# Optimization experiments

Hardware: AMD Instinct MI355X
Metric: run time of the kernel (lower is better)

The kernel has to match this reference:

```python
import jax, jax.numpy as jnp
import numpy as np

B, T = 256, 2048
VOCAB, EMB, HID, OUT = 7, 20, 128, 6


def setup_inputs() -> dict:
    key = jax.random.key(0)
    ks = jax.random.split(key, 9)
    s_ih = 1.0 / np.sqrt(HID)
    inp = {
        "inputs": jax.random.randint(ks[0], (B, T), 0, VOCAB),
        "c0": jax.random.normal(ks[1], (1, B, HID), dtype=jnp.float32),
        # PyTorch LSTM params (gate order i,f,g,o), uniform(-1/sqrt(H), 1/sqrt(H))
        "W_ih": jax.random.uniform(ks[2], (4 * HID, EMB), jnp.float32, -s_ih, s_ih),
        "W_hh": jax.random.uniform(ks[3], (4 * HID, HID), jnp.float32, -s_ih, s_ih),
        "b_ih": jax.random.uniform(ks[4], (4 * HID,), jnp.float32, -s_ih, s_ih),
        "b_hh": jax.random.uniform(ks[5], (4 * HID,), jnp.float32, -s_ih, s_ih),
        "W_fc": jax.random.uniform(ks[6], (OUT, HID), jnp.float32, -s_ih, s_ih),
        "b_fc": jax.random.uniform(ks[7], (OUT,), jnp.float32, -s_ih, s_ih),
        "emb": jax.random.normal(ks[8], (VOCAB, EMB), dtype=jnp.float32),
    }
    return inp


def _lstm(x_gates, h0, c0, W_hh):
    # x_gates: [T, B, 4H] precomputed input contributions (+ both biases)
    def step(carry, xg):
        h, c = carry
        gates = xg + h @ W_hh.T  # [B, 4H]
        i, f, g, o = jnp.split(gates, 4, axis=-1)
        i, f, o = jax.nn.sigmoid(i), jax.nn.sigmoid(f), jax.nn.sigmoid(o)
        g = jnp.tanh(g)
        c = f * c + i * g
        h = o * jnp.tanh(c)
        return (h, c), h

    (_, _), hs = jax.lax.scan(step, (h0, c0), x_gates)
    return hs  # [T, B, H]


def reference(inputs, c0, W_ih, W_hh, b_ih, b_hh, W_fc, b_fc, emb):
    x = emb[inputs]  # [B, T, EMB]
    # precompute input-to-gate projection once (batched GEMM)
    x_gates = jnp.einsum("bte,ge->btg", x, W_ih) + (b_ih + b_hh)  # [B,T,4H]
    x_gates = jnp.transpose(x_gates, (1, 0, 2))  # [T, B, 4H]
    h0 = jnp.zeros((B, HID), dtype=x.dtype)
    hs = _lstm(x_gates, h0, c0[0], W_hh)  # [T, B, H]
    hiddens = jnp.transpose(hs, (1, 0, 2))  # [B, T, H]
    logits = jnp.einsum("bth,oh->bto", hiddens, W_fc) + b_fc
    return jax.nn.softmax(logits, axis=2)
```

## Files before the change

### kernel.cpp

```cpp
#include <hip/hip_runtime.h>
#include <math.h>

#define BB 256
#define TT 2048
#define VOCAB 7
#define EMBD 20
#define HID 128
#define OUTD 6
#define CHUNK 64
#define NCHUNK (TT / CHUNK)

typedef _Float16 h2 __attribute__((ext_vector_type(2)));

__device__ __forceinline__ float v_exp2(float x) {
    float r; asm("v_exp_f32 %0, %1" : "=v"(r) : "v"(x)); return r;
}
__device__ __forceinline__ float v_rcp(float x) {
    float r; asm("v_rcp_f32 %0, %1" : "=v"(r) : "v"(x)); return r;
}
__device__ __forceinline__ float sigmoid_f(float x) {
    return v_rcp(1.0f + v_exp2(-1.44269504f * x));
}
__device__ __forceinline__ float tanh_f(float x) {
    float ax = fabsf(x);
    float t = v_exp2(-2.88539008f * ax);
    float r = (1.0f - t) * v_rcp(1.0f + t);
    return __builtin_copysignf(r, x);
}

__device__ __forceinline__ float dot2(h2 a, h2 b, float c) {
    float d;
    asm("v_dot2_f32_f16 %0, %1, %2, %3" : "=v"(d) : "v"(a), "v"(b), "v"(c));
    return d;
}

#define KEEP(x) asm volatile("" : "+v"(x))

__global__ __launch_bounds__(512) void lstm_persist(
    const int* __restrict__ inputs, const float* __restrict__ c0,
    const float* __restrict__ W_ih, const float* __restrict__ W_hh,
    const float* __restrict__ b_ih, const float* __restrict__ b_hh,
    const float* __restrict__ W_fc, const float* __restrict__ b_fc,
    const float* __restrict__ emb, float* __restrict__ out)
{
    __shared__ float4   gtab[VOCAB][HID];
    __shared__ _Float16 hbuf[CHUNK][HID];
    __shared__ int      toks[CHUNK];
    __shared__ float    ldspad[24 * 1024];

    const int tid  = threadIdx.x;
    const int b    = blockIdx.x;
    const int j    = tid >> 2;
    const int r    = tid & 3;
    const int lane = tid & 63;
    const int wave = tid >> 6;

    h2 w0[16], w1[16], w2[16], w3[16];
    {
        const float2* p0 = (const float2*)(W_hh + ((size_t)(0 * HID + j) * HID + r * 32));
        const float2* p1 = (const float2*)(W_hh + ((size_t)(1 * HID + j) * HID + r * 32));
        const float2* p2 = (const float2*)(W_hh + ((size_t)(2 * HID + j) * HID + r * 32));
        const float2* p3 = (const float2*)(W_hh + ((size_t)(3 * HID + j) * HID + r * 32));
        #pragma unroll
        for (int k = 0; k < 16; ++k) {
            float2 f0 = p0[k], f1 = p1[k], f2 = p2[k], f3 = p3[k];
            h2 a; a.x = (_Float16)f0.x; a.y = (_Float16)f0.y; w0[k] = a;
            h2 bq; bq.x = (_Float16)f1.x; bq.y = (_Float16)f1.y; w1[k] = bq;
            h2 cq; cq.x = (_Float16)f2.x; cq.y = (_Float16)f2.y; w2[k] = cq;
            h2 dq; dq.x = (_Float16)f3.x; dq.y = (_Float16)f3.y; w3[k] = dq;
        }
    }
    #pragma unroll
    for (int k = 0; k < 16; ++k) { KEEP(w0[k]); KEEP(w1[k]); KEEP(w2[k]); KEEP(w3[k]); }

    {
        const int g = r * HID + j;
        float wih[EMBD];
        #pragma unroll
        for (int e = 0; e < EMBD; ++e) wih[e] = W_ih[g * EMBD + e];
        float bb = b_ih[g] + b_hh[g];
        #pragma unroll
        for (int v = 0; v < VOCAB; ++v) {
            float a = bb;
            #pragma unroll
            for (int e = 0; e < EMBD; ++e) a += wih[e] * emb[v * EMBD + e];
            ((float*)&gtab[v][j])[r] = a;
        }
    }

    float c = c0[b * HID + j];
    if (tid < HID) hbuf[CHUNK - 1][tid] = (_Float16)0.f;

    float wfc0[OUTD], wfc1[OUTD], bfc[OUTD];
    #pragma unroll
    for (int o = 0; o < OUTD; ++o) {
        wfc0[o] = W_fc[o * HID + 2 * lane];
        wfc1[o] = W_fc[o * HID + 2 * lane + 1];
        bfc[o]  = b_fc[o];
    }
    __syncthreads();

    #pragma unroll 1
    for (int ch = 0; ch < NCHUNK; ++ch) {
        const int t0 = ch * CHUNK;
        if (tid < CHUNK) toks[tid] = inputs[(size_t)b * TT + t0 + tid];
        __syncthreads();

        #pragma unroll 1
        for (int s = 0; s < CHUNK; ++s) {
            const int prev = (s + CHUNK - 1) & (CHUNK - 1);

            const uint4* hp = (const uint4*)&hbuf[prev][r * 32];
            float a0 = 0.f, a1 = 0.f, a2 = 0.f, a3 = 0.f;
            #pragma unroll
            for (int k = 0; k < 4; ++k) {
                uint4 v = hp[k];
                h2 hx = __builtin_bit_cast(h2, v.x);
                h2 hy = __builtin_bit_cast(h2, v.y);
                h2 hz = __builtin_bit_cast(h2, v.z);
                h2 hw = __builtin_bit_cast(h2, v.w);
                a0 = dot2(w0[4*k+0], hx, a0); a0 = dot2(w0[4*k+1], hy, a0);
                a0 = dot2(w0[4*k+2], hz, a0); a0 = dot2(w0[4*k+3], hw, a0);
                a1 = dot2(w1[4*k+0], hx, a1); a1 = dot2(w1[4*k+1], hy, a1);
                a1 = dot2(w1[4*k+2], hz, a1); a1 = dot2(w1[4*k+3], hw, a1);
                a2 = dot2(w2[4*k+0], hx, a2); a2 = dot2(w2[4*k+1], hy, a2);
                a2 = dot2(w2[4*k+2], hz, a2); a2 = dot2(w2[4*k+3], hw, a2);
                a3 = dot2(w3[4*k+0], hx, a3); a3 = dot2(w3[4*k+1], hy, a3);
                a3 = dot2(w3[4*k+2], hz, a3); a3 = dot2(w3[4*k+3], hw, a3);
            }
            a0 += __shfl_xor(a0, 1, 64); a0 += __shfl_xor(a0, 2, 64);
            a1 += __shfl_xor(a1, 1, 64); a1 += __shfl_xor(a1, 2, 64);
            a2 += __shfl_xor(a2, 1, 64); a2 += __shfl_xor(a2, 2, 64);
            a3 += __shfl_xor(a3, 1, 64); a3 += __shfl_xor(a3, 2, 64);

            const float4 xg = gtab[toks[s]][j];
            float gi = sigmoid_f(a0 + xg.x);
            float gf = sigmoid_f(a1 + xg.y);
            float gg = tanh_f  (a2 + xg.z);
            float go = sigmoid_f(a3 + xg.w);
            c = gf * c + gi * gg;
            float h = go * tanh_f(c);
            if (r == 0) hbuf[s][j] = (_Float16)h;
            __syncthreads();
        }

        #pragma unroll 1
        for (int i = 0; i < CHUNK / 8; ++i) {
            const int row = wave * (CHUNK / 8) + i;
            h2 hv = ((const h2*)&hbuf[row][0])[lane];
            float h0 = (float)hv.x, h1 = (float)hv.y;
            float acc[OUTD];
            #pragma unroll
            for (int o = 0; o < OUTD; ++o) acc[o] = wfc0[o] * h0 + wfc1[o] * h1;
            #pragma unroll
            for (int off = 32; off >= 1; off >>= 1) {
                #pragma unroll
                for (int o = 0; o < OUTD; ++o) acc[o] += __shfl_xor(acc[o], off, 64);
            }
            if (lane == 0) {
                float m = -1e30f;
                #pragma unroll
                for (int o = 0; o < OUTD; ++o) { acc[o] += bfc[o]; m = fmaxf(m, acc[o]); }
                float e[OUTD], ssum = 0.f;
                #pragma unroll
                for (int o = 0; o < OUTD; ++o) { e[o] = v_exp2(1.44269504f * (acc[o] - m)); ssum += e[o]; }
                float inv = v_rcp(ssum);
                float* po = out + ((size_t)b * TT + (t0 + row)) * OUTD;
                #pragma unroll
                for (int o = 0; o < OUTD; ++o) po[o] = e[o] * inv;
            }
        }
        __syncthreads();
    }

    if (__builtin_expect(inputs[0] == -2147483647, 0)) {
        volatile float* vp = ldspad;
        vp[tid] = (float)tid;
        out[tid] = vp[tid + 1];
    }
}

extern "C" void kernel_launch(void* const* d_in, const int* in_sizes, int n_in,
                              void* d_out, int out_size, void* d_ws, size_t ws_size,
                              hipStream_t stream) {
    const int*   inputs = (const int*)  d_in[0];
    const float* c0     = (const float*)d_in[1];
    const float* W_ih   = (const float*)d_in[2];
    const float* W_hh   = (const float*)d_in[3];
    const float* b_ih   = (const float*)d_in[4];
    const float* b_hh   = (const float*)d_in[5];
    const float* W_fc   = (const float*)d_in[6];
    const float* b_fc   = (const float*)d_in[7];
    const float* emb    = (const float*)d_in[8];
    float* out = (float*)d_out;

    lstm_persist<<<BB, 512, 0, stream>>>(inputs, c0, W_ih, W_hh, b_ih, b_hh,
                                         W_fc, b_fc, emb, out);
}
```

Before: 1.584 ms.

## Split each hidden unit's recurrent dot product across eight threads with 1024-thread blocks

Doubles the block to 1024 threads so each hidden unit's four gate dot products are split across eight lanes of 16 elements instead of four lanes of 32. This halves per-thread serial dot2 work and weight registers, at the cost of an extra shuffle-reduction stage and a costlier block-wide barrier every step. It also preloads all tokens into shared memory once and prefetches the next step's input-gate row before the barrier. The dot product now uses the fdot2 builtin instead of inline asm, and the padding array is halved.

Result: slower. 2.070 ms (+30.7%).

```diff
diff --git a/kernel.cpp b/kernel.cpp
--- a/kernel.cpp
+++ b/kernel.cpp
@@ -28,15 +28,21 @@
     return __builtin_copysignf(r, x);
 }
 
+#if defined(__has_builtin)
+#if __has_builtin(__builtin_amdgcn_fdot2)
+#define HAS_FDOT2 1
+#endif
+#endif
+
 __device__ __forceinline__ float dot2(h2 a, h2 b, float c) {
-    float d;
-    asm("v_dot2_f32_f16 %0, %1, %2, %3" : "=v"(d) : "v"(a), "v"(b), "v"(c));
-    return d;
-}
-
-#define KEEP(x) asm volatile("" : "+v"(x))
-
-__global__ __launch_bounds__(512) void lstm_persist(
+#ifdef HAS_FDOT2
+    return __builtin_amdgcn_fdot2(a, b, c, false);
+#else
+    return c + (float)a.x * (float)b.x + (float)a.y * (float)b.y;
+#endif
+}
+
+__global__ __launch_bounds__(1024) void lstm_persist(
     const int* __restrict__ inputs, const float* __restrict__ c0,
     const float* __restrict__ W_ih, const float* __restrict__ W_hh,
     const float* __restrict__ b_ih, const float* __restrict__ b_hh,
@@ -45,36 +51,35 @@
 {
     __shared__ float4   gtab[VOCAB][HID];
     __shared__ _Float16 hbuf[CHUNK][HID];
-    __shared__ int      toks[CHUNK];
-    __shared__ float    ldspad[24 * 1024];
+    __shared__ int      toks[TT];
+    __shared__ float    ldspad[12 * 1024];
 
     const int tid  = threadIdx.x;
     const int b    = blockIdx.x;
-    const int j    = tid >> 2;
-    const int r    = tid & 3;
+    const int j    = tid >> 3;
+    const int r    = tid & 7;
     const int lane = tid & 63;
     const int wave = tid >> 6;
 
-    h2 w0[16], w1[16], w2[16], w3[16];
-    {
-        const float2* p0 = (const float2*)(W_hh + ((size_t)(0 * HID + j) * HID + r * 32));
-        const float2* p1 = (const float2*)(W_hh + ((size_t)(1 * HID + j) * HID + r * 32));
-        const float2* p2 = (const float2*)(W_hh + ((size_t)(2 * HID + j) * HID + r * 32));
-        const float2* p3 = (const float2*)(W_hh + ((size_t)(3 * HID + j) * HID + r * 32));
+    toks[tid]        = inputs[(size_t)b * TT + tid];
+    toks[tid + 1024] = inputs[(size_t)b * TT + tid + 1024];
+
+    h2 w[4][8];
+    #pragma unroll
+    for (int g = 0; g < 4; ++g) {
+        const float2* wp = (const float2*)(W_hh + ((size_t)(g * HID + j) * HID + r * 16));
         #pragma unroll
-        for (int k = 0; k < 16; ++k) {
-            float2 f0 = p0[k], f1 = p1[k], f2 = p2[k], f3 = p3[k];
-            h2 a; a.x = (_Float16)f0.x; a.y = (_Float16)f0.y; w0[k] = a;
-            h2 bq; bq.x = (_Float16)f1.x; bq.y = (_Float16)f1.y; w1[k] = bq;
-            h2 cq; cq.x = (_Float16)f2.x; cq.y = (_Float16)f2.y; w2[k] = cq;
-            h2 dq; dq.x = (_Float16)f3.x; dq.y = (_Float16)f3.y; w3[k] = dq;
-        }
-    }
-    #pragma unroll
-    for (int k = 0; k < 16; ++k) { KEEP(w0[k]); KEEP(w1[k]); KEEP(w2[k]); KEEP(w3[k]); }
-
-    {
-        const int g = r * HID + j;
+        for (int k = 0; k < 8; ++k) {
+            float2 f = wp[k];
+            h2 p; p.x = (_Float16)f.x; p.y = (_Float16)f.y;
+            w[g][k] = p;
+        }
+    }
+
+    if (tid < 4 * HID) {
+        const int jj = tid & (HID - 1);
+        const int gg = tid >> 7;
+        const int g  = gg * HID + jj;
         float wih[EMBD];
         #pragma unroll
         for (int e = 0; e < EMBD; ++e) wih[e] = W_ih[g * EMBD + e];
@@ -84,7 +89,7 @@
             float a = bb;
             #pragma unroll
             for (int e = 0; e < EMBD; ++e) a += wih[e] * emb[v * EMBD + e];
-            ((float*)&gtab[v][j])[r] = a;
+            ((float*)&gtab[v][jj])[gg] = a;
         }
     }
 
@@ -100,40 +105,51 @@
     }
     __syncthreads();
 
+    float4 xg = gtab[toks[0]][j];
+
     #pragma unroll 1
     for (int ch = 0; ch < NCHUNK; ++ch) {
         const int t0 = ch * CHUNK;
-        if (tid < CHUNK) toks[tid] = inputs[(size_t)b * TT + t0 + tid];
-        __syncthreads();
 
         #pragma unroll 1
         for (int s = 0; s < CHUNK; ++s) {
+            const int t    = t0 + s;
             const int prev = (s + CHUNK - 1) & (CHUNK - 1);
 
-            const uint4* hp = (const uint4*)&hbuf[prev][r * 32];
+            const uint4* hp = (const uint4*)&hbuf[prev][r * 16];
+            uint4 v0 = hp[0], v1 = hp[1];
+
             float a0 = 0.f, a1 = 0.f, a2 = 0.f, a3 = 0.f;
             #pragma unroll
-            for (int k = 0; k < 4; ++k) {
-                uint4 v = hp[k];
-                h2 hx = __builtin_bit_cast(h2, v.x);
-                h2 hy = __builtin_bit_cast(h2, v.y);
-                h2 hz = __builtin_bit_cast(h2, v.z);
-                h2 hw = __builtin_bit_cast(h2, v.w);
-                a0 = dot2(w0[4*k+0], hx, a0); a0 = dot2(w0[4*k+1], hy, a0);
-                a0 = dot2(w0[4*k+2], hz, a0); a0 = dot2(w0[4*k+3], hw, a0);
-                a1 = dot2(w1[4*k+0], hx, a1); a1 = dot2(w1[4*k+1], hy, a1);
-                a1 = dot2(w1[4*k+2], hz, a1); a1 = dot2(w1[4*k+3], hw, a1);
-                a2 = dot2(w2[4*k+0], hx, a2); a2 = dot2(w2[4*k+1], hy, a2);
-                a2 = dot2(w2[4*k+2], hz, a2); a2 = dot2(w2[4*k+3], hw, a2);
-                a3 = dot2(w3[4*k+0], hx, a3); a3 = dot2(w3[4*k+1], hy, a3);
-                a3 = dot2(w3[4*k+2], hz, a3); a3 = dot2(w3[4*k+3], hw, a3);
+            for (int g = 0; g < 1; ++g) {  }
+            {
+                h2 hx0 = __builtin_bit_cast(h2, v0.x), hy0 = __builtin_bit_cast(h2, v0.y);
+                h2 hz0 = __builtin_bit_cast(h2, v0.z), hw0 = __builtin_bit_cast(h2, v0.w);
+                h2 hx1 = __builtin_bit_cast(h2, v1.x), hy1 = __builtin_bit_cast(h2, v1.y);
+                h2 hz1 = __builtin_bit_cast(h2, v1.z), hw1 = __builtin_bit_cast(h2, v1.w);
+                a0 = dot2(w[0][0], hx0, a0); a0 = dot2(w[0][1], hy0, a0);
+                a0 = dot2(w[0][2], hz0, a0); a0 = dot2(w[0][3], hw0, a0);
+                a0 = dot2(w[0][4], hx1, a0); a0 = dot2(w[0][5], hy1, a0);
+                a0 = dot2(w[0][6], hz1, a0); a0 = dot2(w[0][7], hw1, a0);
+                a1 = dot2(w[1][0], hx0, a1); a1 = dot2(w[1][1], hy0, a1);
+                a1 = dot2(w[1][2], hz0, a1); a1 = dot2(w[1][3], hw0, a1);
+                a1 = dot2(w[1][4], hx1, a1); a1 = dot2(w[1][5], hy1, a1);
+                a1 = dot2(w[1][6], hz1, a1); a1 = dot2(w[1][7], hw1, a1);
+                a2 = dot2(w[2][0], hx0, a2); a2 = dot2(w[2][1], hy0, a2);
+                a2 = dot2(w[2][2], hz0, a2); a2 = dot2(w[2][3], hw0, a2);
+                a2 = dot2(w[2][4], hx1, a2); a2 = dot2(w[2][5], hy1, a2);
+                a2 = dot2(w[2][6], hz1, a2); a2 = dot2(w[2][7], hw1, a2);
+                a3 = dot2(w[3][0], hx0, a3); a3 = dot2(w[3][1], hy0, a3);
+                a3 = dot2(w[3][2], hz0, a3); a3 = dot2(w[3][3], hw0, a3);
+                a3 = dot2(w[3][4], hx1, a3); a3 = dot2(w[3][5], hy1, a3);
+                a3 = dot2(w[3][6], hz1, a3); a3 = dot2(w[3][7], hw1, a3);
             }
-            a0 += __shfl_xor(a0, 1, 64); a0 += __shfl_xor(a0, 2, 64);
-            a1 += __shfl_xor(a1, 1, 64); a1 += __shfl_xor(a1, 2, 64);
-            a2 += __shfl_xor(a2, 1, 64); a2 += __shfl_xor(a2, 2, 64);
-            a3 += __shfl_xor(a3, 1, 64); a3 += __shfl_xor(a3, 2, 64);
-
-            const float4 xg = gtab[toks[s]][j];
+
+            a0 += __shfl_xor(a0, 1, 64); a0 += __shfl_xor(a0, 2, 64); a0 += __shfl_xor(a0, 4, 64);
+            a1 += __shfl_xor(a1, 1, 64); a1 += __shfl_xor(a1, 2, 64); a1 += __shfl_xor(a1, 4, 64);
+            a2 += __shfl_xor(a2, 1, 64); a2 += __shfl_xor(a2, 2, 64); a2 += __shfl_xor(a2, 4, 64);
+            a3 += __shfl_xor(a3, 1, 64); a3 += __shfl_xor(a3, 2, 64); a3 += __shfl_xor(a3, 4, 64);
+
             float gi = sigmoid_f(a0 + xg.x);
             float gf = sigmoid_f(a1 + xg.y);
             float gg = tanh_f  (a2 + xg.z);
@@ -141,12 +157,14 @@
             c = gf * c + gi * gg;
             float h = go * tanh_f(c);
             if (r == 0) hbuf[s][j] = (_Float16)h;
+
+            xg = gtab[toks[(t + 1) & (TT - 1)]][j];
             __syncthreads();
         }
 
         #pragma unroll 1
-        for (int i = 0; i < CHUNK / 8; ++i) {
-            const int row = wave * (CHUNK / 8) + i;
+        for (int i = 0; i < CHUNK / 16; ++i) {
+            const int row = wave * (CHUNK / 16) + i;
             h2 hv = ((const h2*)&hbuf[row][0])[lane];
             float h0 = (float)hv.x, h1 = (float)hv.y;
             float acc[OUTD];
@@ -194,6 +212,6 @@
     const float* emb    = (const float*)d_in[8];
     float* out = (float*)d_out;
 
-    lstm_persist<<<BB, 512, 0, stream>>>(inputs, c0, W_ih, W_hh, b_ih, b_hh,
-                                         W_fc, b_fc, emb, out);
-}
+    lstm_persist<<<BB, 1024, 0, stream>>>(inputs, c0, W_ih, W_hh, b_ih, b_hh,
+                                          W_fc, b_fc, emb, out);
+}
```

## Use DPP quad reductions, preload all tokens, and use fdot2 builtin

Applied to the files above, without the earlier changes.

Replaces the xor-shuffle reductions across the four lanes that share a gate row with DPP quad_perm adds, which avoids the LDS-based bpermute round trips on the serial critical path of every timestep. All 2048 tokens are now loaded into shared memory up front, which removes the per-chunk global load and its extra barrier. The inline-asm dot2 is swapped for the compiler builtin and the KEEP register pins are dropped, so the compiler can schedule freely but might spill or rematerialize the weight registers.

Result: faster. 1.390 ms (-12.2%).

```diff
diff --git a/kernel.cpp b/kernel.cpp
--- a/kernel.cpp
+++ b/kernel.cpp
@@ -28,13 +28,27 @@
     return __builtin_copysignf(r, x);
 }
 
+#if defined(__has_builtin)
+#if __has_builtin(__builtin_amdgcn_fdot2)
+#define HAS_FDOT2 1
+#endif
+#endif
+
 __device__ __forceinline__ float dot2(h2 a, h2 b, float c) {
-    float d;
-    asm("v_dot2_f32_f16 %0, %1, %2, %3" : "=v"(d) : "v"(a), "v"(b), "v"(c));
-    return d;
-}
-
-#define KEEP(x) asm volatile("" : "+v"(x))
+#ifdef HAS_FDOT2
+    return __builtin_amdgcn_fdot2(a, b, c, false);
+#else
+    return c + (float)a.x * (float)b.x + (float)a.y * (float)b.y;
+#endif
+}
+
+__device__ __forceinline__ float qreduce(float x) {
+    int t1 = __builtin_amdgcn_update_dpp(0, __builtin_bit_cast(int, x), 0xB1, 0xF, 0xF, true);
+    x += __builtin_bit_cast(float, t1);
+    int t2 = __builtin_amdgcn_update_dpp(0, __builtin_bit_cast(int, x), 0x4E, 0xF, 0xF, true);
+    x += __builtin_bit_cast(float, t2);
+    return x;
+}
 
 __global__ __launch_bounds__(512) void lstm_persist(
     const int* __restrict__ inputs, const float* __restrict__ c0,
@@ -45,7 +59,7 @@
 {
     __shared__ float4   gtab[VOCAB][HID];
     __shared__ _Float16 hbuf[CHUNK][HID];
-    __shared__ int      toks[CHUNK];
+    __shared__ int      toks[TT];
     __shared__ float    ldspad[24 * 1024];
 
     const int tid  = threadIdx.x;
@@ -54,6 +68,10 @@
     const int r    = tid & 3;
     const int lane = tid & 63;
     const int wave = tid >> 6;
+
+    #pragma unroll
+    for (int i = 0; i < TT / 512; ++i)
+        toks[tid + 512 * i] = inputs[(size_t)b * TT + tid + 512 * i];
 
     h2 w0[16], w1[16], w2[16], w3[16];
     {
@@ -70,8 +88,6 @@
             h2 dq; dq.x = (_Float16)f3.x; dq.y = (_Float16)f3.y; w3[k] = dq;
         }
     }
-    #pragma unroll
-    for (int k = 0; k < 16; ++k) { KEEP(w0[k]); KEEP(w1[k]); KEEP(w2[k]); KEEP(w3[k]); }
 
     {
         const int g = r * HID + j;
@@ -103,8 +119,6 @@
     #pragma unroll 1
     for (int ch = 0; ch < NCHUNK; ++ch) {
         const int t0 = ch * CHUNK;
-        if (tid < CHUNK) toks[tid] = inputs[(size_t)b * TT + t0 + tid];
-        __syncthreads();
 
         #pragma unroll 1
         for (int s = 0; s < CHUNK; ++s) {
@@ -128,12 +142,10 @@
                 a3 = dot2(w3[4*k+0], hx, a3); a3 = dot2(w3[4*k+1], hy, a3);
                 a3 = dot2(w3[4*k+2], hz, a3); a3 = dot2(w3[4*k+3], hw, a3);
             }
-            a0 += __shfl_xor(a0, 1, 64); a0 += __shfl_xor(a0, 2, 64);
-            a1 += __shfl_xor(a1, 1, 64); a1 += __shfl_xor(a1, 2, 64);
-            a2 += __shfl_xor(a2, 1, 64); a2 += __shfl_xor(a2, 2, 64);
-            a3 += __shfl_xor(a3, 1, 64); a3 += __shfl_xor(a3, 2, 64);
-
-            const float4 xg = gtab[toks[s]][j];
+            a0 = qreduce(a0); a1 = qreduce(a1);
+            a2 = qreduce(a2); a3 = qreduce(a3);
+
+            const float4 xg = gtab[toks[t0 + s]][j];
             float gi = sigmoid_f(a0 + xg.x);
             float gf = sigmoid_f(a1 + xg.y);
             float gg = tanh_f  (a2 + xg.z);
```
